# Performance work log

Measured on AMD Instinct MI355X. Metric: run time of the kernel, lower is better.

Reference implementation:

```python
import jax, jax.numpy as jnp
import numpy as np

N = 65536        # nodes
E = 1048576      # edges (avg degree 16)
F_IN = 128
H = 64
OUT = 32
L = 3            # num conv layers
EPS = 1e-5


def layernorm(x, g, b):
    m = jnp.mean(x, axis=-1, keepdims=True)
    v = jnp.mean(jnp.square(x - m), axis=-1, keepdims=True)
    return (x - m) * jax.lax.rsqrt(v + EPS) * g + b


def setup_inputs() -> dict:
    key = jax.random.key(0)
    ks = jax.random.split(key, 16)
    s1 = 1.0 / np.sqrt(F_IN)
    s2 = 1.0 / np.sqrt(H)
    return {
        "x": jax.random.normal(ks[0], (N, F_IN), jnp.float32),
        "edge_weight": jax.random.uniform(ks[1], (E, 1), jnp.float32),
        "src": jax.random.randint(ks[2], (E,), 0, N, jnp.int32),
        "dst": jax.random.randint(ks[3], (E,), 0, N, jnp.int32),
        # fc_first: LayerNorm(F_IN) -> Linear(F_IN,H) -> ELU
        "ln1_g": jnp.ones((F_IN,), jnp.float32),
        "ln1_b": jnp.zeros((F_IN,), jnp.float32),
        "w1": jax.random.uniform(ks[4], (F_IN, H), jnp.float32, -s1, s1),
        "b1": jax.random.uniform(ks[5], (H,), jnp.float32, -s1, s1),
        # shared LayerNorm(H)
        "ln_g": jnp.ones((H,), jnp.float32),
        "ln_b": jnp.zeros((H,), jnp.float32),
        # L GraphConvolution layers (H -> H)
        "conv_w": jax.random.uniform(ks[6], (L, H, H), jnp.float32, -s2, s2),
        "conv_b": jax.random.uniform(ks[7], (L, H), jnp.float32, -s2, s2),
        # fc_final: LayerNorm(H) -> Linear(H,H) -> ELU -> Linear(H,OUT)
        "ln2_g": jnp.ones((H,), jnp.float32),
        "ln2_b": jnp.zeros((H,), jnp.float32),
        "w3": jax.random.uniform(ks[8], (H, H), jnp.float32, -s2, s2),
        "b3": jax.random.uniform(ks[9], (H,), jnp.float32, -s2, s2),
        "w4": jax.random.uniform(ks[10], (H, OUT), jnp.float32, -s2, s2),
        "b4": jax.random.uniform(ks[11], (OUT,), jnp.float32, -s2, s2),
    }


def reference(x, edge_weight, src, dst, ln1_g, ln1_b, w1, b1, ln_g, ln_b,
              conv_w, conv_b, ln2_g, ln2_b, w3, b3, w4, b4):
    # fc_first (dropout p=0 is identity in eval)
    h = jax.nn.elu(layernorm(x, ln1_g, ln1_b) @ w1 + b1)
    h = layernorm(h, ln_g, ln_b)                       # [N, H]
    res_sum = h                                        # running sum of `hiddens`
    for i in range(L):
        # u_mul_e + sum: gather src features, scale by edge weight, scatter-add at dst
        msg = h[src] * edge_weight                     # [E, H]
        agg = jax.ops.segment_sum(msg, dst, num_segments=N)  # [N, H]
        h = layernorm(agg @ conv_w[i] + conv_b[i], ln_g, ln_b)
        cur = h
        h = h + res_sum                                # add all previous hiddens
        res_sum = res_sum + cur
    # fc_final
    z = jax.nn.elu(layernorm(h, ln2_g, ln2_b) @ w3 + b3)
    return z @ w4 + b4                                 # [N, OUT]
```

## Files before the change

### kernel.cpp

```cpp
#include <hip/hip_runtime.h>

#define NN   65536
#define NE   1048576
#define CAP  48
#define NP   512
#define NODP 128
#define PCAP 2560
#define FIN  128
#define HD   64
#define NOUT 32
#define EPSV 1e-5f

typedef unsigned short u16;
typedef unsigned int u32;
typedef __attribute__((ext_vector_type(8))) short short8v;
typedef __attribute__((ext_vector_type(4))) float f32x4;

__device__ __forceinline__ u16 f2bf(float f) {
  u32 x = __float_as_uint(f);
  u32 r = x + 0x7FFFu + ((x >> 16) & 1u);
  return (u16)(r >> 16);
}
__device__ __forceinline__ float bf2f(u16 u) {
  return __uint_as_float((u32)u << 16);
}

__device__ __forceinline__ void fma4bf(float4& acc, uint2 g, float w) {
  acc.x += __uint_as_float(g.x << 16) * w;
  acc.y += __uint_as_float(g.x & 0xFFFF0000u) * w;
  acc.z += __uint_as_float(g.y << 16) * w;
  acc.w += __uint_as_float(g.y & 0xFFFF0000u) * w;
}

__global__ __launch_bounds__(512) void zero_k(int* __restrict__ pcnt) {
  pcnt[threadIdx.x] = 0;
}

__global__ __launch_bounds__(1024) void passA_k(
    const int* __restrict__ src, const int* __restrict__ dst,
    const float* __restrict__ ew, int* __restrict__ pcnt,
    uint2* __restrict__ tmp) {
  __shared__ int hist[NP];
  __shared__ int base[NP];
  int t = threadIdx.x;
  if (t < NP) hist[t] = 0;
  __syncthreads();

  int d[4], s[4];
  float w[4];
  size_t e0 = (size_t)blockIdx.x * 4096;
#pragma unroll
  for (int r = 0; r < 4; ++r) {
    int i = e0 + r * 1024 + t;
    d[r] = dst[i]; s[r] = src[i]; w[r] = ew[i];
    atomicAdd(&hist[d[r] >> 7], 1);
  }
  __syncthreads();
  if (t < NP) {
    int c = hist[t];
    base[t] = c ? atomicAdd(&pcnt[t], c) : 0;
    hist[t] = 0;
  }
  __syncthreads();
#pragma unroll
  for (int r = 0; r < 4; ++r) {
    int bin = d[r] >> 7;
    int pos = base[bin] + atomicAdd(&hist[bin], 1);
    if (pos < PCAP)
      tmp[(size_t)bin * PCAP + pos] =
          make_uint2(((u32)d[r] << 16) | (u32)s[r], __float_as_uint(w[r]));
  }
}

__global__ __launch_bounds__(256) void passB_k(
    const uint2* __restrict__ tmp, const int* __restrict__ pcnt,
    u32* __restrict__ edgep, int* __restrict__ ecnt) {
  __shared__ int cur[NODP];
  int p = blockIdx.x, t = threadIdx.x;
  if (t < NODP) cur[t] = 0;
  __syncthreads();
  int cntp = min(pcnt[p], PCAP);
  const uint2* tp = tmp + (size_t)p * PCAP;
  for (int i = t; i < cntp; i += 256) {
    uint2 e = tp[i];
    int dd = e.x >> 16;
    int pos = atomicAdd(&cur[dd & (NODP - 1)], 1);
    if (pos < CAP)
      edgep[(size_t)dd * CAP + pos] =
          (e.x & 0xFFFFu) | ((u32)f2bf(__uint_as_float(e.y)) << 16);
  }
  __syncthreads();
  if (t < NODP) {
    int node = p * NODP + t;
    int c = min(cur[t], CAP);
    int padded = min((c + 3) & ~3, CAP);
    for (int s = c; s < padded; ++s)
      edgep[(size_t)node * CAP + s] = 0u;
    ecnt[node] = padded;
  }
}

__global__ __launch_bounds__(256, 4) void fc_first_k(
    const float* __restrict__ x, const float* __restrict__ ln1_g,
    const float* __restrict__ ln1_b, const float* __restrict__ w1,
    const float* __restrict__ b1, const float* __restrict__ ln_g,
    const float* __restrict__ ln_b, u16* __restrict__ hAbf) {
  __shared__ __align__(16) u16 sXn[64 * 136];
  __shared__ __align__(16) u16 sWb[64 * 136];
  __shared__ __align__(16) float sG[FIN], sB[FIN];
  int tid = threadIdx.x;
  for (int i = tid; i < FIN * HD; i += 256) {
    int k = i >> 6, j = i & 63;
    sWb[j * 136 + k] = f2bf(w1[i]);
  }
  if (tid < FIN) { sG[tid] = ln1_g[tid]; sB[tid] = ln1_b[tid]; }
  __syncthreads();

  {
    int jq = tid & 3;
    int nl = tid >> 2;
    int node = blockIdx.x * 64 + nl;
    const float4* xp = (const float4*)(x + (size_t)node * FIN + jq * 32);
    float xv[32];
    float s = 0.f, s2 = 0.f;
#pragma unroll
    for (int i = 0; i < 8; ++i) {
      float4 v = xp[i];
      xv[i * 4 + 0] = v.x; xv[i * 4 + 1] = v.y;
      xv[i * 4 + 2] = v.z; xv[i * 4 + 3] = v.w;
      s += v.x + v.y + v.z + v.w;
      s2 += v.x * v.x + v.y * v.y + v.z * v.z + v.w * v.w;
    }
    s += __shfl_xor(s, 1, 64);  s += __shfl_xor(s, 2, 64);
    s2 += __shfl_xor(s2, 1, 64); s2 += __shfl_xor(s2, 2, 64);
    float mean = s * (1.f / FIN);
    float var = s2 * (1.f / FIN) - mean * mean;
    float r = rsqrtf(var + EPSV);
    u32* dp = (u32*)&sXn[nl * 136 + jq * 32];
#pragma unroll
    for (int i = 0; i < 16; ++i) {
      int k = jq * 32 + i * 2;
      float a0 = (xv[i * 2 + 0] - mean) * r * sG[k + 0] + sB[k + 0];
      float a1 = (xv[i * 2 + 1] - mean) * r * sG[k + 1] + sB[k + 1];
      dp[i] = (u32)f2bf(a0) | ((u32)f2bf(a1) << 16);
    }
  }
  __syncthreads();

  int wl = tid >> 6, lane = tid & 63;
  int q = lane >> 4, fq = lane & 15;
  f32x4 d0 = {0.f, 0.f, 0.f, 0.f}, d1 = d0, d2 = d0, d3 = d0;
#pragma unroll
  for (int st = 0; st < 4; ++st) {
    short8v av = *(const short8v*)&sXn[(wl * 16 + fq) * 136 + st * 32 + q * 8];
    short8v b0 = *(const short8v*)&sWb[(0 * 16 + fq) * 136 + st * 32 + q * 8];
    short8v b1v = *(const short8v*)&sWb[(1 * 16 + fq) * 136 + st * 32 + q * 8];
    short8v b2 = *(const short8v*)&sWb[(2 * 16 + fq) * 136 + st * 32 + q * 8];
    short8v b3v = *(const short8v*)&sWb[(3 * 16 + fq) * 136 + st * 32 + q * 8];
    d0 = __builtin_amdgcn_mfma_f32_16x16x32_bf16(av, b0, d0, 0, 0, 0);
    d1 = __builtin_amdgcn_mfma_f32_16x16x32_bf16(av, b1v, d1, 0, 0, 0);
    d2 = __builtin_amdgcn_mfma_f32_16x16x32_bf16(av, b2, d2, 0, 0, 0);
    d3 = __builtin_amdgcn_mfma_f32_16x16x32_bf16(av, b3v, d3, 0, 0, 0);
  }

  float b1r[4], lgr[4], lbr[4];
#pragma unroll
  for (int t = 0; t < 4; ++t) {
    b1r[t] = b1[t * 16 + fq];
    lgr[t] = ln_g[t * 16 + fq];
    lbr[t] = ln_b[t * 16 + fq];
  }
  float y0[4], y1[4], y2[4], y3[4];
  float ps[4], ps2[4];
#pragma unroll
  for (int reg = 0; reg < 4; ++reg) {
    float v0 = d0[reg] + b1r[0]; v0 = (v0 > 0.f) ? v0 : expm1f(v0);
    float v1 = d1[reg] + b1r[1]; v1 = (v1 > 0.f) ? v1 : expm1f(v1);
    float v2 = d2[reg] + b1r[2]; v2 = (v2 > 0.f) ? v2 : expm1f(v2);
    float v3 = d3[reg] + b1r[3]; v3 = (v3 > 0.f) ? v3 : expm1f(v3);
    y0[reg] = v0; y1[reg] = v1; y2[reg] = v2; y3[reg] = v3;
    ps[reg] = v0 + v1 + v2 + v3;
    ps2[reg] = v0 * v0 + v1 * v1 + v2 * v2 + v3 * v3;
  }
#pragma unroll
  for (int o = 1; o <= 8; o <<= 1) {
#pragma unroll
    for (int reg = 0; reg < 4; ++reg) {
      ps[reg] += __shfl_xor(ps[reg], o, 64);
      ps2[reg] += __shfl_xor(ps2[reg], o, 64);
    }
  }
#pragma unroll
  for (int reg = 0; reg < 4; ++reg) {
    int n = blockIdx.x * 64 + wl * 16 + q * 4 + reg;
    float m2 = ps[reg] * (1.f / HD);
    float vv = ps2[reg] * (1.f / HD) - m2 * m2;
    float r2 = rsqrtf(vv + EPSV);
    hAbf[(size_t)n * HD + 0 * 16 + fq] = f2bf((y0[reg] - m2) * r2 * lgr[0] + lbr[0]);
    hAbf[(size_t)n * HD + 1 * 16 + fq] = f2bf((y1[reg] - m2) * r2 * lgr[1] + lbr[1]);
    hAbf[(size_t)n * HD + 2 * 16 + fq] = f2bf((y2[reg] - m2) * r2 * lgr[2] + lbr[2]);
    hAbf[(size_t)n * HD + 3 * 16 + fq] = f2bf((y3[reg] - m2) * r2 * lgr[3] + lbr[3]);
  }
}

__global__ __launch_bounds__(512, 8) void conv_k(
    const u16* __restrict__ hbf_in, u16* __restrict__ hbf_out,
    const int* __restrict__ ecnt, const u32* __restrict__ edgep,
    const float* __restrict__ W, const float* __restrict__ B,
    const float* __restrict__ ln_g, const float* __restrict__ ln_b) {
  __shared__ __align__(16) u16 sWt[HD * 72];
  __shared__ __align__(16) u16 sAgg[32 * 72];
  __shared__ __align__(16) float sOut[32 * 68];
  int tid = threadIdx.x;
  for (int i = tid; i < HD * HD; i += 512) {
    int k = i >> 6, j = i & 63;
    sWt[j * 72 + k] = f2bf(W[i]);
  }

  int wl = tid >> 6, lane = tid & 63;
  int q = lane >> 4;
  int fq = lane & 15;
  int nbase = blockIdx.x * 32;

  int cntR[4];
  u32 HR[4];
#pragma unroll
  for (int rp = 0; rp < 4; ++rp) {
    int n = nbase + wl * 4 + rp;
    cntR[rp] = ecnt[n];
    HR[rp] = edgep[(size_t)n * CAP + min(lane, 31)];
  }

#pragma unroll
  for (int rp = 0; rp < 4; ++rp) {
    int n = nbase + wl * 4 + rp;
    int cnt = cntR[rp];
    u32 H = HR[rp];

    float4 acc = make_float4(0.f, 0.f, 0.f, 0.f);
    if (cnt > 0) {
      int ng = cnt >> 2;
      int ngs = min(ng, 8);
      int g = 0;
      for (; g + 4 <= ngs; g += 4) {
        u32 h0 = __shfl(H, (g + 0) * 4 + q, 64);
        u32 h1 = __shfl(H, (g + 1) * 4 + q, 64);
        u32 h2 = __shfl(H, (g + 2) * 4 + q, 64);
        u32 h3 = __shfl(H, (g + 3) * 4 + q, 64);
        uint2 g0 = ((const uint2*)(hbf_in + ((size_t)(h0 & 0xFFFFu) << 6)))[fq];
        uint2 g1 = ((const uint2*)(hbf_in + ((size_t)(h1 & 0xFFFFu) << 6)))[fq];
        uint2 g2 = ((const uint2*)(hbf_in + ((size_t)(h2 & 0xFFFFu) << 6)))[fq];
        uint2 g3 = ((const uint2*)(hbf_in + ((size_t)(h3 & 0xFFFFu) << 6)))[fq];
        fma4bf(acc, g0, __uint_as_float(h0 & 0xFFFF0000u));
        fma4bf(acc, g1, __uint_as_float(h1 & 0xFFFF0000u));
        fma4bf(acc, g2, __uint_as_float(h2 & 0xFFFF0000u));
        fma4bf(acc, g3, __uint_as_float(h3 & 0xFFFF0000u));
      }
      for (; g < ngs; ++g) {
        u32 hj = __shfl(H, g * 4 + q, 64);
        uint2 gg = ((const uint2*)(hbf_in + ((size_t)(hj & 0xFFFFu) << 6)))[fq];
        fma4bf(acc, gg, __uint_as_float(hj & 0xFFFF0000u));
      }
      for (; g < ng; ++g) {
        u32 hj = edgep[(size_t)n * CAP + g * 4 + q];
        uint2 gg = ((const uint2*)(hbf_in + ((size_t)(hj & 0xFFFFu) << 6)))[fq];
        fma4bf(acc, gg, __uint_as_float(hj & 0xFFFF0000u));
      }
    }
#pragma unroll
    for (int off = 16; off < 64; off <<= 1) {
      acc.x += __shfl_xor(acc.x, off, 64);
      acc.y += __shfl_xor(acc.y, off, 64);
      acc.z += __shfl_xor(acc.z, off, 64);
      acc.w += __shfl_xor(acc.w, off, 64);
    }
    if (lane < 16) {
      u32 p0 = (u32)f2bf(acc.x) | ((u32)f2bf(acc.y) << 16);
      u32 p1 = (u32)f2bf(acc.z) | ((u32)f2bf(acc.w) << 16);
      u32* dp = (u32*)&sAgg[(wl * 4 + rp) * 72 + fq * 4];
      dp[0] = p0; dp[1] = p1;
    }
  }
  __syncthreads();

  {
    int g = wl >> 2, t = wl & 3;
    f32x4 d = {0.f, 0.f, 0.f, 0.f};
#pragma unroll
    for (int s = 0; s < 2; ++s) {
      short8v av = *(const short8v*)&sAgg[(g * 16 + fq) * 72 + s * 32 + q * 8];
      short8v bv = *(const short8v*)&sWt[(t * 16 + fq) * 72 + s * 32 + q * 8];
      d = __builtin_amdgcn_mfma_f32_16x16x32_bf16(av, bv, d, 0, 0, 0);
    }
#pragma unroll
    for (int reg = 0; reg < 4; ++reg) {
      int row = q * 4 + reg;
      sOut[(g * 16 + row) * 68 + t * 16 + fq] = d[reg];
    }
  }
  __syncthreads();

  float bias = B[lane], lg = ln_g[lane], lb = ln_b[lane];
#pragma unroll
  for (int rp = 0; rp < 4; ++rp) {
    int nl = wl * 4 + rp;
    int n = nbase + nl;
    float y = sOut[nl * 68 + lane] + bias;
    float a = y, b2 = y * y;
#pragma unroll
    for (int o = 32; o > 0; o >>= 1) {
      a += __shfl_xor(a, o, 64);
      b2 += __shfl_xor(b2, o, 64);
    }
    float m = a * (1.f / HD);
    float v = b2 * (1.f / HD) - m * m;
    float ln = (y - m) * rsqrtf(v + EPSV) * lg + lb;
    float hv = bf2f(hbf_in[(size_t)n * HD + lane]) + ln;
    hbf_out[(size_t)n * HD + lane] = f2bf(hv);
  }
}

__global__ __launch_bounds__(256, 4) void fc_final_k(
    const u16* __restrict__ hbf, const float* __restrict__ ln2_g,
    const float* __restrict__ ln2_b, const float* __restrict__ w3,
    const float* __restrict__ b3, const float* __restrict__ w4,
    const float* __restrict__ b4, float* __restrict__ out) {
  __shared__ __align__(16) float sW3[HD * HD];
  __shared__ __align__(16) float sW4[HD * NOUT];
  __shared__ __align__(16) float sG[HD], sB[HD], sB3[HD], sB4[NOUT];
  int tid = threadIdx.x;
  {
    const float4* a = (const float4*)w3;
    float4* d4 = (float4*)sW3;
    for (int i = tid; i < HD * HD / 4; i += 256) d4[i] = a[i];
    const float4* c = (const float4*)w4;
    float4* e4 = (float4*)sW4;
    for (int i = tid; i < HD * NOUT / 4; i += 256) e4[i] = c[i];
    if (tid < HD) { sG[tid] = ln2_g[tid]; sB[tid] = ln2_b[tid]; sB3[tid] = b3[tid]; }
    if (tid < NOUT) sB4[tid] = b4[tid];
  }
  __syncthreads();

  int jq = tid & 3;
  int node = blockIdx.x * 64 + (tid >> 2);
  const u32* hr = (const u32*)(hbf + (size_t)node * HD);

  float s = 0.f, s2 = 0.f;
  for (int i = 0; i < 8; ++i) {
    uint4 v = ((const uint4*)hr)[i];
    float f0 = __uint_as_float(v.x << 16), f1 = __uint_as_float(v.x & 0xFFFF0000u);
    float f2 = __uint_as_float(v.y << 16), f3 = __uint_as_float(v.y & 0xFFFF0000u);
    float f4 = __uint_as_float(v.z << 16), f5 = __uint_as_float(v.z & 0xFFFF0000u);
    float f6 = __uint_as_float(v.w << 16), f7 = __uint_as_float(v.w & 0xFFFF0000u);
    s += f0 + f1 + f2 + f3 + f4 + f5 + f6 + f7;
    s2 += f0 * f0 + f1 * f1 + f2 * f2 + f3 * f3
        + f4 * f4 + f5 * f5 + f6 * f6 + f7 * f7;
  }
  float mean = s * (1.f / HD);
  float var = s2 * (1.f / HD) - mean * mean;
  float r = rsqrtf(var + EPSV);

  float acc[16];
#pragma unroll
  for (int jb = 0; jb < 4; ++jb) {
    float4 b = ((const float4*)sB3)[jq * 4 + jb];
    acc[jb * 4 + 0] = b.x; acc[jb * 4 + 1] = b.y;
    acc[jb * 4 + 2] = b.z; acc[jb * 4 + 3] = b.w;
  }
  const float4* sW34 = (const float4*)sW3;
  for (int k4 = 0; k4 < HD / 4; ++k4) {
    uint2 rw = ((const uint2*)hr)[k4];
    float xk0 = __uint_as_float(rw.x << 16);
    float xk1 = __uint_as_float(rw.x & 0xFFFF0000u);
    float xk2 = __uint_as_float(rw.y << 16);
    float xk3 = __uint_as_float(rw.y & 0xFFFF0000u);
    float4 g4 = ((const float4*)sG)[k4];
    float4 bb4 = ((const float4*)sB)[k4];
    float xn0 = (xk0 - mean) * r * g4.x + bb4.x;
    float xn1 = (xk1 - mean) * r * g4.y + bb4.y;
    float xn2 = (xk2 - mean) * r * g4.z + bb4.z;
    float xn3 = (xk3 - mean) * r * g4.w + bb4.w;
#pragma unroll
    for (int jb = 0; jb < 4; ++jb) {
      float4 w0 = sW34[(k4 * 4 + 0) * 16 + jq * 4 + jb];
      float4 w1v = sW34[(k4 * 4 + 1) * 16 + jq * 4 + jb];
      float4 w2 = sW34[(k4 * 4 + 2) * 16 + jq * 4 + jb];
      float4 w3v = sW34[(k4 * 4 + 3) * 16 + jq * 4 + jb];
      acc[jb * 4 + 0] += xn0 * w0.x + xn1 * w1v.x + xn2 * w2.x + xn3 * w3v.x;
      acc[jb * 4 + 1] += xn0 * w0.y + xn1 * w1v.y + xn2 * w2.y + xn3 * w3v.y;
      acc[jb * 4 + 2] += xn0 * w0.z + xn1 * w1v.z + xn2 * w2.z + xn3 * w3v.z;
      acc[jb * 4 + 3] += xn0 * w0.w + xn1 * w1v.w + xn2 * w2.w + xn3 * w3v.w;
    }
  }

#pragma unroll
  for (int j = 0; j < 16; ++j) {
    float y = acc[j];
    acc[j] = (y > 0.f) ? y : expm1f(y);
  }

  const float4* sW44 = (const float4*)sW4;
#pragma unroll
  for (int c = 0; c < 2; ++c) {
    float p[16];
#pragma unroll
    for (int i = 0; i < 16; ++i) p[i] = 0.f;
#pragma unroll
    for (int kk = 0; kk < 16; ++kk) {
      float zk = acc[kk];
      int krow = jq * 16 + kk;
#pragma unroll
      for (int qd = 0; qd < 4; ++qd) {
        float4 w = sW44[krow * 8 + c * 4 + qd];
        p[qd * 4 + 0] += zk * w.x;
        p[qd * 4 + 1] += zk * w.y;
        p[qd * 4 + 2] += zk * w.z;
        p[qd * 4 + 3] += zk * w.w;
      }
    }
#pragma unroll
    for (int i = 0; i < 16; ++i) {
      p[i] += __shfl_xor(p[i], 1, 64);
      p[i] += __shfl_xor(p[i], 2, 64);
    }
    if (jq == c) {
      float4* op = (float4*)(out + (size_t)node * NOUT + c * 16);
#pragma unroll
      for (int qd = 0; qd < 4; ++qd) {
        float4 b = ((const float4*)sB4)[c * 4 + qd];
        float4 o;
        o.x = p[qd * 4 + 0] + b.x; o.y = p[qd * 4 + 1] + b.y;
        o.z = p[qd * 4 + 2] + b.z; o.w = p[qd * 4 + 3] + b.w;
        op[qd] = o;
      }
    }
  }
}

extern "C" void kernel_launch(void* const* d_in, const int* in_sizes, int n_in,
                              void* d_out, int out_size, void* d_ws, size_t ws_size,
                              hipStream_t stream) {
  const float* x      = (const float*)d_in[0];
  const float* ew     = (const float*)d_in[1];
  const int*   src    = (const int*)d_in[2];
  const int*   dst    = (const int*)d_in[3];
  const float* ln1_g  = (const float*)d_in[4];
  const float* ln1_b  = (const float*)d_in[5];
  const float* w1     = (const float*)d_in[6];
  const float* b1     = (const float*)d_in[7];
  const float* ln_g   = (const float*)d_in[8];
  const float* ln_b   = (const float*)d_in[9];
  const float* conv_w = (const float*)d_in[10];
  const float* conv_b = (const float*)d_in[11];
  const float* ln2_g  = (const float*)d_in[12];
  const float* ln2_b  = (const float*)d_in[13];
  const float* w3     = (const float*)d_in[14];
  const float* b3     = (const float*)d_in[15];
  const float* w4     = (const float*)d_in[16];
  const float* b4     = (const float*)d_in[17];
  float* out = (float*)d_out;

  char* ws = (char*)d_ws;
  u16*   hAbf  = (u16*)ws;
  u16*   hBbf  = hAbf + (size_t)NN * HD;
  int*   ecnt  = (int*)(hBbf + (size_t)NN * HD);
  u32*   edgep = (u32*)(ecnt + NN + 64);
  int*   pcnt  = (int*)(edgep + (size_t)NN * CAP);
  uint2* tmp   = (uint2*)(pcnt + NP + 64);

  zero_k<<<1, NP, 0, stream>>>(pcnt);
  passA_k<<<NE / 4096, 1024, 0, stream>>>(src, dst, ew, pcnt, tmp);
  passB_k<<<NP, 256, 0, stream>>>(tmp, pcnt, edgep, ecnt);

  fc_first_k<<<NN / 64, 256, 0, stream>>>(x, ln1_g, ln1_b, w1, b1, ln_g, ln_b,
                                          hAbf);
  conv_k<<<NN / 32, 512, 0, stream>>>(hAbf, hBbf, ecnt, edgep,
                                      conv_w,        conv_b,       ln_g, ln_b);
  conv_k<<<NN / 32, 512, 0, stream>>>(hBbf, hAbf, ecnt, edgep,
                                      conv_w + 4096, conv_b + 64,  ln_g, ln_b);
  conv_k<<<NN / 32, 512, 0, stream>>>(hAbf, hBbf, ecnt, edgep,
                                      conv_w + 8192, conv_b + 128, ln_g, ln_b);
  fc_final_k<<<NN / 64, 256, 0, stream>>>(hBbf, ln2_g, ln2_b, w3, b3, w4, b4, out);
}
```

Baseline: 170.6 us.

## Use bf16 MFMA for fc_final matmuls with LDS-staged normalized activations

Rewrites the fc_final kernel so the LayerNorm output is written as bf16 into shared memory, and both dense layers (HxH then HxOUT) run on 16x16x32 bf16 MFMA instructions instead of scalar FMA loops. Weights are converted to bf16 and transposed into padded LDS tiles. The row reduction is split across four lanes with shuffles. This cuts ALU work in the final stage but adds bf16 rounding of the weights and intermediate activations. It also reloads and converts the weights in every block, and the output stores are now scalar.

```diff
diff --git a/kernel.cpp b/kernel.cpp
--- a/kernel.cpp
+++ b/kernel.cpp
@@ -325,114 +325,105 @@
     const float* __restrict__ ln2_b, const float* __restrict__ w3,
     const float* __restrict__ b3, const float* __restrict__ w4,
     const float* __restrict__ b4, float* __restrict__ out) {
-  __shared__ __align__(16) float sW3[HD * HD];
-  __shared__ __align__(16) float sW4[HD * NOUT];
-  __shared__ __align__(16) float sG[HD], sB[HD], sB3[HD], sB4[NOUT];
+  __shared__ __align__(16) u16 sHn[64 * 72];
+  __shared__ __align__(16) u16 sW3b[64 * 72];
+  __shared__ __align__(16) u16 sW4b[32 * 72];
+  __shared__ __align__(16) u16 sZ[64 * 72];
   int tid = threadIdx.x;
+  for (int i = tid; i < HD * HD; i += 256) {
+    int k = i >> 6, j = i & 63;
+    sW3b[j * 72 + k] = f2bf(w3[i]);
+  }
+  for (int i = tid; i < HD * NOUT; i += 256) {
+    int k = i >> 5, j = i & 31;
+    sW4b[j * 72 + k] = f2bf(w4[i]);
+  }
+
   {
-    const float4* a = (const float4*)w3;
-    float4* d4 = (float4*)sW3;
-    for (int i = tid; i < HD * HD / 4; i += 256) d4[i] = a[i];
-    const float4* c = (const float4*)w4;
-    float4* e4 = (float4*)sW4;
-    for (int i = tid; i < HD * NOUT / 4; i += 256) e4[i] = c[i];
-    if (tid < HD) { sG[tid] = ln2_g[tid]; sB[tid] = ln2_b[tid]; sB3[tid] = b3[tid]; }
-    if (tid < NOUT) sB4[tid] = b4[tid];
-  }
-  __syncthreads();
-
-  int jq = tid & 3;
-  int node = blockIdx.x * 64 + (tid >> 2);
-  const u32* hr = (const u32*)(hbf + (size_t)node * HD);
-
-  float s = 0.f, s2 = 0.f;
-  for (int i = 0; i < 8; ++i) {
-    uint4 v = ((const uint4*)hr)[i];
-    float f0 = __uint_as_float(v.x << 16), f1 = __uint_as_float(v.x & 0xFFFF0000u);
-    float f2 = __uint_as_float(v.y << 16), f3 = __uint_as_float(v.y & 0xFFFF0000u);
-    float f4 = __uint_as_float(v.z << 16), f5 = __uint_as_float(v.z & 0xFFFF0000u);
-    float f6 = __uint_as_float(v.w << 16), f7 = __uint_as_float(v.w & 0xFFFF0000u);
-    s += f0 + f1 + f2 + f3 + f4 + f5 + f6 + f7;
-    s2 += f0 * f0 + f1 * f1 + f2 * f2 + f3 * f3
-        + f4 * f4 + f5 * f5 + f6 * f6 + f7 * f7;
-  }
-  float mean = s * (1.f / HD);
-  float var = s2 * (1.f / HD) - mean * mean;
-  float r = rsqrtf(var + EPSV);
-
-  float acc[16];
-#pragma unroll
-  for (int jb = 0; jb < 4; ++jb) {
-    float4 b = ((const float4*)sB3)[jq * 4 + jb];
-    acc[jb * 4 + 0] = b.x; acc[jb * 4 + 1] = b.y;
-    acc[jb * 4 + 2] = b.z; acc[jb * 4 + 3] = b.w;
-  }
-  const float4* sW34 = (const float4*)sW3;
-  for (int k4 = 0; k4 < HD / 4; ++k4) {
-    uint2 rw = ((const uint2*)hr)[k4];
-    float xk0 = __uint_as_float(rw.x << 16);
-    float xk1 = __uint_as_float(rw.x & 0xFFFF0000u);
-    float xk2 = __uint_as_float(rw.y << 16);
-    float xk3 = __uint_as_float(rw.y & 0xFFFF0000u);
-    float4 g4 = ((const float4*)sG)[k4];
-    float4 bb4 = ((const float4*)sB)[k4];
-    float xn0 = (xk0 - mean) * r * g4.x + bb4.x;
-    float xn1 = (xk1 - mean) * r * g4.y + bb4.y;
-    float xn2 = (xk2 - mean) * r * g4.z + bb4.z;
-    float xn3 = (xk3 - mean) * r * g4.w + bb4.w;
-#pragma unroll
-    for (int jb = 0; jb < 4; ++jb) {
-      float4 w0 = sW34[(k4 * 4 + 0) * 16 + jq * 4 + jb];
-      float4 w1v = sW34[(k4 * 4 + 1) * 16 + jq * 4 + jb];
-      float4 w2 = sW34[(k4 * 4 + 2) * 16 + jq * 4 + jb];
-      float4 w3v = sW34[(k4 * 4 + 3) * 16 + jq * 4 + jb];
-      acc[jb * 4 + 0] += xn0 * w0.x + xn1 * w1v.x + xn2 * w2.x + xn3 * w3v.x;
-      acc[jb * 4 + 1] += xn0 * w0.y + xn1 * w1v.y + xn2 * w2.y + xn3 * w3v.y;
-      acc[jb * 4 + 2] += xn0 * w0.z + xn1 * w1v.z + xn2 * w2.z + xn3 * w3v.z;
-      acc[jb * 4 + 3] += xn0 * w0.w + xn1 * w1v.w + xn2 * w2.w + xn3 * w3v.w;
-    }
-  }
-
-#pragma unroll
-  for (int j = 0; j < 16; ++j) {
-    float y = acc[j];
-    acc[j] = (y > 0.f) ? y : expm1f(y);
-  }
-
-  const float4* sW44 = (const float4*)sW4;
-#pragma unroll
-  for (int c = 0; c < 2; ++c) {
-    float p[16];
-#pragma unroll
-    for (int i = 0; i < 16; ++i) p[i] = 0.f;
-#pragma unroll
-    for (int kk = 0; kk < 16; ++kk) {
-      float zk = acc[kk];
-      int krow = jq * 16 + kk;
-#pragma unroll
-      for (int qd = 0; qd < 4; ++qd) {
-        float4 w = sW44[krow * 8 + c * 4 + qd];
-        p[qd * 4 + 0] += zk * w.x;
-        p[qd * 4 + 1] += zk * w.y;
-        p[qd * 4 + 2] += zk * w.z;
-        p[qd * 4 + 3] += zk * w.w;
-      }
-    }
-#pragma unroll
-    for (int i = 0; i < 16; ++i) {
-      p[i] += __shfl_xor(p[i], 1, 64);
-      p[i] += __shfl_xor(p[i], 2, 64);
-    }
-    if (jq == c) {
-      float4* op = (float4*)(out + (size_t)node * NOUT + c * 16);
-#pragma unroll
-      for (int qd = 0; qd < 4; ++qd) {
-        float4 b = ((const float4*)sB4)[c * 4 + qd];
-        float4 o;
-        o.x = p[qd * 4 + 0] + b.x; o.y = p[qd * 4 + 1] + b.y;
-        o.z = p[qd * 4 + 2] + b.z; o.w = p[qd * 4 + 3] + b.w;
-        op[qd] = o;
-      }
+    int jq = tid & 3;
+    int nl = tid >> 2;
+    int node = blockIdx.x * 64 + nl;
+    const uint4* hp = (const uint4*)(hbf + (size_t)node * HD + jq * 16);
+    float hv[16];
+    float s = 0.f, s2 = 0.f;
+#pragma unroll
+    for (int i = 0; i < 2; ++i) {
+      uint4 v = hp[i];
+      float f0 = __uint_as_float(v.x << 16), f1 = __uint_as_float(v.x & 0xFFFF0000u);
+      float f2 = __uint_as_float(v.y << 16), f3 = __uint_as_float(v.y & 0xFFFF0000u);
+      float f4 = __uint_as_float(v.z << 16), f5 = __uint_as_float(v.z & 0xFFFF0000u);
+      float f6 = __uint_as_float(v.w << 16), f7 = __uint_as_float(v.w & 0xFFFF0000u);
+      hv[i * 8 + 0] = f0; hv[i * 8 + 1] = f1; hv[i * 8 + 2] = f2; hv[i * 8 + 3] = f3;
+      hv[i * 8 + 4] = f4; hv[i * 8 + 5] = f5; hv[i * 8 + 6] = f6; hv[i * 8 + 7] = f7;
+      s += f0 + f1 + f2 + f3 + f4 + f5 + f6 + f7;
+      s2 += f0 * f0 + f1 * f1 + f2 * f2 + f3 * f3
+          + f4 * f4 + f5 * f5 + f6 * f6 + f7 * f7;
+    }
+    s += __shfl_xor(s, 1, 64);  s += __shfl_xor(s, 2, 64);
+    s2 += __shfl_xor(s2, 1, 64); s2 += __shfl_xor(s2, 2, 64);
+    float mean = s * (1.f / HD);
+    float var = s2 * (1.f / HD) - mean * mean;
+    float r = rsqrtf(var + EPSV);
+    u32* dp = (u32*)&sHn[nl * 72 + jq * 16];
+#pragma unroll
+    for (int i = 0; i < 8; ++i) {
+      int k = jq * 16 + i * 2;
+      float a0 = (hv[i * 2 + 0] - mean) * r * ln2_g[k + 0] + ln2_b[k + 0];
+      float a1 = (hv[i * 2 + 1] - mean) * r * ln2_g[k + 1] + ln2_b[k + 1];
+      dp[i] = (u32)f2bf(a0) | ((u32)f2bf(a1) << 16);
+    }
+  }
+  __syncthreads();
+
+  int wl = tid >> 6, lane = tid & 63;
+  int q = lane >> 4, fq = lane & 15;
+  f32x4 d0 = {0.f, 0.f, 0.f, 0.f}, d1 = d0, d2 = d0, d3 = d0;
+#pragma unroll
+  for (int st = 0; st < 2; ++st) {
+    short8v av = *(const short8v*)&sHn[(wl * 16 + fq) * 72 + st * 32 + q * 8];
+    short8v b0 = *(const short8v*)&sW3b[(0 * 16 + fq) * 72 + st * 32 + q * 8];
+    short8v b1v = *(const short8v*)&sW3b[(1 * 16 + fq) * 72 + st * 32 + q * 8];
+    short8v b2 = *(const short8v*)&sW3b[(2 * 16 + fq) * 72 + st * 32 + q * 8];
+    short8v b3v = *(const short8v*)&sW3b[(3 * 16 + fq) * 72 + st * 32 + q * 8];
+    d0 = __builtin_amdgcn_mfma_f32_16x16x32_bf16(av, b0, d0, 0, 0, 0);
+    d1 = __builtin_amdgcn_mfma_f32_16x16x32_bf16(av, b1v, d1, 0, 0, 0);
+    d2 = __builtin_amdgcn_mfma_f32_16x16x32_bf16(av, b2, d2, 0, 0, 0);
+    d3 = __builtin_amdgcn_mfma_f32_16x16x32_bf16(av, b3v, d3, 0, 0, 0);
+  }
+  {
+    float b3r[4];
+#pragma unroll
+    for (int t = 0; t < 4; ++t) b3r[t] = b3[t * 16 + fq];
+#pragma unroll
+    for (int reg = 0; reg < 4; ++reg) {
+      int row = wl * 16 + q * 4 + reg;
+      float v0 = d0[reg] + b3r[0]; v0 = (v0 > 0.f) ? v0 : expm1f(v0);
+      float v1 = d1[reg] + b3r[1]; v1 = (v1 > 0.f) ? v1 : expm1f(v1);
+      float v2 = d2[reg] + b3r[2]; v2 = (v2 > 0.f) ? v2 : expm1f(v2);
+      float v3 = d3[reg] + b3r[3]; v3 = (v3 > 0.f) ? v3 : expm1f(v3);
+      sZ[row * 72 + 0 * 16 + fq] = f2bf(v0);
+      sZ[row * 72 + 1 * 16 + fq] = f2bf(v1);
+      sZ[row * 72 + 2 * 16 + fq] = f2bf(v2);
+      sZ[row * 72 + 3 * 16 + fq] = f2bf(v3);
+    }
+  }
+
+  {
+    f32x4 e0 = {0.f, 0.f, 0.f, 0.f}, e1 = e0;
+#pragma unroll
+    for (int st = 0; st < 2; ++st) {
+      short8v av = *(const short8v*)&sZ[(wl * 16 + fq) * 72 + st * 32 + q * 8];
+      short8v b0 = *(const short8v*)&sW4b[(0 * 16 + fq) * 72 + st * 32 + q * 8];
+      short8v b1v = *(const short8v*)&sW4b[(1 * 16 + fq) * 72 + st * 32 + q * 8];
+      e0 = __builtin_amdgcn_mfma_f32_16x16x32_bf16(av, b0, e0, 0, 0, 0);
+      e1 = __builtin_amdgcn_mfma_f32_16x16x32_bf16(av, b1v, e1, 0, 0, 0);
+    }
+    float b4r0 = b4[0 * 16 + fq], b4r1 = b4[1 * 16 + fq];
+#pragma unroll
+    for (int reg = 0; reg < 4; ++reg) {
+      int n = blockIdx.x * 64 + wl * 16 + q * 4 + reg;
+      out[(size_t)n * NOUT + 0 * 16 + fq] = e0[reg] + b4r0;
+      out[(size_t)n * NOUT + 1 * 16 + fq] = e1[reg] + b4r1;
     }
   }
 }
```

New measurement: 147.6 us. -13.5%, faster.
